# Kernel optimization log

Hardware: AMD Instinct MI355X
Metric: run time of the kernel (lower is better)

The kernel has to match this reference:

```python
import jax, jax.numpy as jnp
import numpy as np

N, E = 50000, 800000
IN_DIM, HEADS, OUT_DIM = 256, 8, 32
NEG_SLOPE = 0.2  # PyG GATConv default leaky_relu slope
LN_EPS = 1e-5


def setup_inputs() -> dict:
    key = jax.random.key(0)
    ks = jax.random.split(key, 8)
    HC = HEADS * OUT_DIM
    x = jax.random.normal(ks[0], (N, IN_DIM), dtype=jnp.float32)
    edge_index = jax.random.randint(ks[1], (2, E), 0, N, dtype=jnp.int32)
    # GATConv params: lin (no bias), att_src/att_dst [H,C], output bias [H*C]
    W = jax.random.normal(ks[2], (IN_DIM, HC), dtype=jnp.float32) / np.sqrt(IN_DIM)
    att_src = jax.random.normal(ks[3], (HEADS, OUT_DIM), dtype=jnp.float32) / np.sqrt(OUT_DIM)
    att_dst = jax.random.normal(ks[4], (HEADS, OUT_DIM), dtype=jnp.float32) / np.sqrt(OUT_DIM)
    bias = jnp.zeros((HC,), dtype=jnp.float32)
    ln_gamma = jnp.ones((HC,), dtype=jnp.float32)
    ln_beta = jnp.zeros((HC,), dtype=jnp.float32)
    return {"x": x, "edge_index": edge_index, "W": W, "att_src": att_src,
            "att_dst": att_dst, "bias": bias, "ln_gamma": ln_gamma, "ln_beta": ln_beta}


def reference(x, edge_index, W, att_src, att_dst, bias, ln_gamma, ln_beta):
    n = x.shape[0]
    # GATConv adds self-loops by default
    loop = jnp.arange(n, dtype=edge_index.dtype)
    src = jnp.concatenate([edge_index[0], loop])  # [E+N]
    dst = jnp.concatenate([edge_index[1], loop])
    h = (x @ W).reshape(n, HEADS, OUT_DIM)              # [N,H,C]
    a_src = jnp.einsum('nhc,hc->nh', h, att_src)        # [N,H]
    a_dst = jnp.einsum('nhc,hc->nh', h, att_dst)
    e = jax.nn.leaky_relu(a_src[src] + a_dst[dst], NEG_SLOPE)  # [E+N,H]
    # segment-softmax over incoming edges of each destination node
    m = jax.ops.segment_max(e, dst, num_segments=n)
    e = jnp.exp(e - m[dst])
    denom = jax.ops.segment_sum(e, dst, num_segments=n)
    alpha = e / (denom[dst] + 1e-16)                    # [E+N,H]
    out = jax.ops.segment_sum(h[src] * alpha[:, :, None], dst, num_segments=n)
    out = out.reshape(n, HEADS * OUT_DIM) + bias        # concat heads + bias
    # LayerNorm(out_dim*heads); dropout is identity in eval
    mu = jnp.mean(out, axis=-1, keepdims=True)
    var = jnp.mean(jnp.square(out - mu), axis=-1, keepdims=True)
    return ln_gamma * (out - mu) * jax.lax.rsqrt(var + LN_EPS) + ln_beta
```

## Files before the change

### kernel.cpp

```cpp
#include <hip/hip_runtime.h>

#define HEADS 8
#define OUT_DIM 32
#define HC 256
#define IN_DIM 256
#define NEG_SLOPE 0.2f
#define LN_EPS 1e-5f
#define CAP 64

typedef __attribute__((ext_vector_type(8))) short bf16x8;
typedef __attribute__((ext_vector_type(4))) float f32x4;
typedef __attribute__((ext_vector_type(2))) float f32x2;

__device__ __forceinline__ unsigned short f2bf(float f) {
    unsigned int u = __float_as_uint(f);
    unsigned int r = u + 0x7FFFu + ((u >> 16) & 1u);
    return (unsigned short)(r >> 16);
}
__device__ __forceinline__ float bf2f(unsigned short u) {
    return __uint_as_float((unsigned int)u << 16);
}

__global__ __launch_bounds__(256) void cast_wT(const float* __restrict__ W,
                                               unsigned short* __restrict__ Wt) {
    __shared__ float tile[64][65];
    const int n0 = (blockIdx.x & 3) * 64;
    const int k0 = (blockIdx.x >> 2) * 64;
    const int t = threadIdx.x;
    const int r = t >> 4;
    const int c = (t & 15) * 4;
#pragma unroll
    for (int j = 0; j < 4; j++) {
        const int kl = r + j * 16;
        const float4 v = *(const float4*)(W + (size_t)(k0 + kl) * HC + n0 + c);
        tile[kl][c + 0] = v.x; tile[kl][c + 1] = v.y;
        tile[kl][c + 2] = v.z; tile[kl][c + 3] = v.w;
    }
    __syncthreads();
#pragma unroll
    for (int j = 0; j < 4; j++) {
        const int nr = r + j * 16;
        ushort4 o;
        o.x = f2bf(tile[c + 0][nr]);
        o.y = f2bf(tile[c + 1][nr]);
        o.z = f2bf(tile[c + 2][nr]);
        o.w = f2bf(tile[c + 3][nr]);
        *(ushort4*)(Wt + (size_t)(n0 + nr) * IN_DIM + k0 + c) = o;
    }
}

__global__ __launch_bounds__(256) void gemm_bf16(const float* __restrict__ X,
                                                 const unsigned short* __restrict__ Wt,
                                                 unsigned short* __restrict__ Hb,
                                                 const float* __restrict__ att_s,
                                                 const float* __restrict__ att_d,
                                                 float* __restrict__ a_s,
                                                 float* __restrict__ a_d, int M) {
    __shared__ unsigned short smem[128 * 40 + 256 * 40];
    unsigned short* As = smem;
    unsigned short* Bs = smem + 128 * 40;
    const int t = threadIdx.x;
    const int m0 = blockIdx.x * 128;
    const int w = t >> 6, lane = t & 63;
    const int wr = w >> 1, wn = w & 1;
    const int l16 = lane & 15, quad = lane >> 4;

    f32x4 acc[4][8] = {};

    for (int k0 = 0; k0 < IN_DIM; k0 += 32) {
#pragma unroll
        for (int j = 0; j < 4; j++) {
            const int idx = t + j * 256;
            const int row = idx >> 3;
            const int part = idx & 7;
            float4 v = make_float4(0.f, 0.f, 0.f, 0.f);
            const int gm = m0 + row;
            if (gm < M) v = *(const float4*)(X + (size_t)gm * IN_DIM + k0 + part * 4);
            ushort4 b;
            b.x = f2bf(v.x); b.y = f2bf(v.y); b.z = f2bf(v.z); b.w = f2bf(v.w);
            *(ushort4*)&As[row * 40 + part * 4] = b;
        }
#pragma unroll
        for (int j = 0; j < 4; j++) {
            const int idx = t + j * 256;
            const int n = idx >> 2;
            const int part = idx & 3;
            *(uint4*)&Bs[n * 40 + part * 8] =
                *(const uint4*)(Wt + (size_t)n * IN_DIM + k0 + part * 8);
        }
        __syncthreads();

        bf16x8 af[4];
#pragma unroll
        for (int mi = 0; mi < 4; mi++) {
            const int row = wr * 64 + mi * 16 + l16;
            af[mi] = *(const bf16x8*)&As[row * 40 + quad * 8];
        }
#pragma unroll
        for (int ni = 0; ni < 8; ni++) {
            const int col = wn * 128 + ni * 16 + l16;
            const bf16x8 bfr = *(const bf16x8*)&Bs[col * 40 + quad * 8];
#pragma unroll
            for (int mi = 0; mi < 4; mi++)
                acc[mi][ni] = __builtin_amdgcn_mfma_f32_16x16x32_bf16(af[mi], bfr, acc[mi][ni], 0, 0, 0);
        }
        __syncthreads();
    }

    {
        float as_v[8], ad_v[8];
#pragma unroll
        for (int ni = 0; ni < 8; ni++) {
            as_v[ni] = att_s[wn * 128 + ni * 16 + l16];
            ad_v[ni] = att_d[wn * 128 + ni * 16 + l16];
        }
#pragma unroll
        for (int mi = 0; mi < 4; mi++) {
#pragma unroll
            for (int reg = 0; reg < 4; reg++) {
                float ps0 = acc[mi][0][reg] * as_v[0] + acc[mi][1][reg] * as_v[1];
                float ps1 = acc[mi][2][reg] * as_v[2] + acc[mi][3][reg] * as_v[3];
                float ps2 = acc[mi][4][reg] * as_v[4] + acc[mi][5][reg] * as_v[5];
                float ps3 = acc[mi][6][reg] * as_v[6] + acc[mi][7][reg] * as_v[7];
                float pd0 = acc[mi][0][reg] * ad_v[0] + acc[mi][1][reg] * ad_v[1];
                float pd1 = acc[mi][2][reg] * ad_v[2] + acc[mi][3][reg] * ad_v[3];
                float pd2 = acc[mi][4][reg] * ad_v[4] + acc[mi][5][reg] * ad_v[5];
                float pd3 = acc[mi][6][reg] * ad_v[6] + acc[mi][7][reg] * ad_v[7];
#pragma unroll
                for (int m = 1; m <= 2; m <<= 1) {
                    ps0 += __shfl_xor(ps0, m); ps1 += __shfl_xor(ps1, m);
                    ps2 += __shfl_xor(ps2, m); ps3 += __shfl_xor(ps3, m);
                    pd0 += __shfl_xor(pd0, m); pd1 += __shfl_xor(pd1, m);
                    pd2 += __shfl_xor(pd2, m); pd3 += __shfl_xor(pd3, m);
                }
                const int s2 = l16 & 3;
                float vs = s2 == 0 ? ps0 : (s2 == 1 ? ps1 : (s2 == 2 ? ps2 : ps3));
                float vd = s2 == 0 ? pd0 : (s2 == 1 ? pd1 : (s2 == 2 ? pd2 : pd3));
                vs += __shfl_xor(vs, 4); vs += __shfl_xor(vs, 8);
                vd += __shfl_xor(vd, 4); vd += __shfl_xor(vd, 8);
                const int gm = m0 + wr * 64 + mi * 16 + quad * 4 + reg;
                if (l16 < 4 && gm < M) {
                    a_s[(size_t)gm * HEADS + wn * 4 + l16] = vs;
                    a_d[(size_t)gm * HEADS + wn * 4 + l16] = vd;
                }
            }
        }
    }

    unsigned short* cbuf = smem + w * 2048;
#pragma unroll
    for (int mi = 0; mi < 4; mi++) {
#pragma unroll
        for (int ni = 0; ni < 8; ni++) {
#pragma unroll
            for (int reg = 0; reg < 4; reg++) {
                cbuf[(quad * 4 + reg) * 128 + ni * 16 + l16] = f2bf(acc[mi][ni][reg]);
            }
        }
#pragma unroll
        for (int j = 0; j < 4; j++) {
            const int q = lane + 64 * j;
            const int r = q >> 4;
            const int cc = q & 15;
            const uint4 v = *(const uint4*)&cbuf[r * 128 + cc * 8];
            const int gm = m0 + wr * 64 + mi * 16 + r;
            if (gm < M)
                *(uint4*)(Hb + (size_t)gm * HC + wn * 128 + cc * 8) = v;
        }
    }
}

__global__ __launch_bounds__(256) void bucket_scatter(const int* __restrict__ ei,
                                                      int* __restrict__ cnt,
                                                      int* __restrict__ bucket,
                                                      int E, int N) {
    const int e = blockIdx.x * 256 + threadIdx.x;
    if (e >= E + N) return;
    int s, d;
    if (e < E) { s = ei[e]; d = ei[E + e]; }
    else       { s = d = e - E; }
    int slot = atomicAdd(&cnt[d], 1);
    if (slot < CAP) bucket[(size_t)d * CAP + slot] = s;
}

__global__ __launch_bounds__(256) void csr_agg(const int* __restrict__ cntArr,
                                               const int* __restrict__ bucket,
                                               const unsigned short* __restrict__ Hb,
                                               const float* __restrict__ a_s,
                                               const float* __restrict__ a_d,
                                               const float* __restrict__ bias,
                                               const float* __restrict__ gamma,
                                               const float* __restrict__ beta,
                                               float* __restrict__ out, int N) {
    const int lane = threadIdx.x & 63;
    const int node = blockIdx.x * 4 + (threadIdx.x >> 6);
    if (node >= N) return;
    const int half = lane >> 5;
    const int sl   = lane & 31;
    const int c0   = sl * 8;
    const int hh   = sl >> 2;
    const int base = node * CAP;
    const int cnt  = min(cntArr[node], CAP);
    const float adv = a_d[(size_t)node * HEADS + hh];
    const int breg = bucket[base + lane];

    f32x2 acc2[4] = {};
    float wsum = 0.f;

    const int nIter = (cnt + 7) >> 3;

    int   sv[4];  float tl[4];  float msk[4];  uint4 hv[4];
#pragma unroll
    for (int j = 0; j < 4; j++) {
        const int idx = 2 * j + half;
        const int s = __shfl(breg, idx);
        const bool ok = idx < cnt;
        sv[j]  = ok ? s : 0;
        msk[j] = ok ? 1.f : 0.f;
    }
#pragma unroll
    for (int j = 0; j < 4; j++) tl[j] = a_s[(size_t)sv[j] * HEADS + hh];
#pragma unroll
    for (int j = 0; j < 4; j++) hv[j] = *(const uint4*)(Hb + (size_t)sv[j] * HC + c0);

    for (int it = 0; it < nIter; ++it) {
        int   sv2[4]; float tl2[4]; float msk2[4]; uint4 hv2[4];
        const int i2 = (it + 1) * 8;
#pragma unroll
        for (int j = 0; j < 4; j++) {
            const int idx = i2 + 2 * j + half;
            const int s = __shfl(breg, idx & 63);
            const bool ok = idx < cnt;
            sv2[j]  = ok ? s : 0;
            msk2[j] = ok ? 1.f : 0.f;
        }
#pragma unroll
        for (int j = 0; j < 4; j++) tl2[j] = a_s[(size_t)sv2[j] * HEADS + hh];
#pragma unroll
        for (int j = 0; j < 4; j++) hv2[j] = *(const uint4*)(Hb + (size_t)sv2[j] * HC + c0);

#pragma unroll
        for (int j = 0; j < 4; j++) {
            const float t = tl[j] + adv;
            const float l = fmaxf(t, NEG_SLOPE * t);
            const float w = msk[j] * __expf(l);
            wsum += w;
            f32x2 wv; wv.x = w; wv.y = w;
            f32x2 p0, p1, p2, p3;
            p0.x = __uint_as_float(hv[j].x << 16); p0.y = __uint_as_float(hv[j].x & 0xffff0000u);
            p1.x = __uint_as_float(hv[j].y << 16); p1.y = __uint_as_float(hv[j].y & 0xffff0000u);
            p2.x = __uint_as_float(hv[j].z << 16); p2.y = __uint_as_float(hv[j].z & 0xffff0000u);
            p3.x = __uint_as_float(hv[j].w << 16); p3.y = __uint_as_float(hv[j].w & 0xffff0000u);
            acc2[0] += wv * p0;
            acc2[1] += wv * p1;
            acc2[2] += wv * p2;
            acc2[3] += wv * p3;
        }
#pragma unroll
        for (int j = 0; j < 4; j++) { tl[j] = tl2[j]; msk[j] = msk2[j]; hv[j] = hv2[j]; }
    }

    float acc[8];
    acc[0] = acc2[0].x; acc[1] = acc2[0].y; acc[2] = acc2[1].x; acc[3] = acc2[1].y;
    acc[4] = acc2[2].x; acc[5] = acc2[2].y; acc[6] = acc2[3].x; acc[7] = acc2[3].y;

#pragma unroll
    for (int k = 0; k < 8; k++) acc[k] += __shfl_xor(acc[k], 32);
    wsum += __shfl_xor(wsum, 32);

    const float inv = 1.f / (wsum + 1e-16f);
    const float4 b0 = *(const float4*)(bias + c0);
    const float4 b1 = *(const float4*)(bias + c0 + 4);
    float v[8];
    v[0] = acc[0] * inv + b0.x; v[1] = acc[1] * inv + b0.y;
    v[2] = acc[2] * inv + b0.z; v[3] = acc[3] * inv + b0.w;
    v[4] = acc[4] * inv + b1.x; v[5] = acc[5] * inv + b1.y;
    v[6] = acc[6] * inv + b1.z; v[7] = acc[7] * inv + b1.w;

    float s1 = v[0] + v[1] + v[2] + v[3] + v[4] + v[5] + v[6] + v[7];
#pragma unroll
    for (int m = 1; m < 64; m <<= 1) s1 += __shfl_xor(s1, m);
    const float mu = s1 * (1.f / 512.f);
    float d[8];
    float sq = 0.f;
#pragma unroll
    for (int k = 0; k < 8; k++) { d[k] = v[k] - mu; sq += d[k] * d[k]; }
#pragma unroll
    for (int m = 1; m < 64; m <<= 1) sq += __shfl_xor(sq, m);
    const float rs = rsqrtf(sq * (1.f / 512.f) + LN_EPS);

    const float e0 = half ? d[4] : d[0];
    const float e1 = half ? d[5] : d[1];
    const float e2 = half ? d[6] : d[2];
    const float e3 = half ? d[7] : d[3];
    const int co = c0 + half * 4;
    const float4 g  = *(const float4*)(gamma + co);
    const float4 be = *(const float4*)(beta + co);
    float4 o;
    o.x = g.x * e0 * rs + be.x;
    o.y = g.y * e1 * rs + be.y;
    o.z = g.z * e2 * rs + be.z;
    o.w = g.w * e3 * rs + be.w;
    *(float4*)(out + (size_t)node * HC + co) = o;
}

extern "C" void kernel_launch(void* const* d_in, const int* in_sizes, int n_in,
                              void* d_out, int out_size, void* d_ws, size_t ws_size,
                              hipStream_t stream) {
    const float* x     = (const float*)d_in[0];
    const int*   ei    = (const int*)d_in[1];
    const float* W     = (const float*)d_in[2];
    const float* att_s = (const float*)d_in[3];
    const float* att_d = (const float*)d_in[4];
    const float* bias  = (const float*)d_in[5];
    const float* gamma = (const float*)d_in[6];
    const float* beta  = (const float*)d_in[7];
    float* out = (float*)d_out;

    const int N = in_sizes[0] / IN_DIM;
    const int E = in_sizes[1] / 2;
    const int tot = E + N;

    unsigned short* Hb = (unsigned short*)d_ws;
    unsigned short* Wt = Hb + (size_t)N * HC;
    float* a_s  = (float*)(Wt + (size_t)IN_DIM * HC);
    float* a_d  = a_s + (size_t)N * HEADS;
    int* cnt    = (int*)(a_d + (size_t)N * HEADS);
    int* bucket = cnt + N;

    hipMemsetAsync(cnt, 0, (size_t)N * sizeof(int), stream);

    bucket_scatter<<<(tot + 255) / 256, 256, 0, stream>>>(ei, cnt, bucket, E, N);
    cast_wT<<<16, 256, 0, stream>>>(W, Wt);
    gemm_bf16<<<(N + 127) / 128, 256, 0, stream>>>(x, Wt, Hb, att_s, att_d, a_s, a_d, N);

    csr_agg<<<(N + 3) / 4, 256, 0, stream>>>(cnt, bucket, Hb, a_s, a_d,
                                             bias, gamma, beta, out, N);
}
```

Before: 287.1 us.

## Drop LDS staging in GEMM and compute attention logits in separate kernel

The GEMM now loads X and W fragments straight from global memory into MFMA registers with no shared memory or barriers, uses 64-row tiles with 4 waves each covering 64 columns, and writes bf16 H directly. The attention dot products a_s and a_d move out of the GEMM epilogue into a new node_att kernel that rereads the bf16 H. This aims to cut barrier and LDS overhead and register pressure to raise occupancy. The cost is redundant global loads of X across waves, uncoalesced scalar stores of H, an extra launch, and logits computed from bf16-rounded H rather than fp32 accumulators.

```diff
diff --git a/kernel.cpp b/kernel.cpp
--- a/kernel.cpp
+++ b/kernel.cpp
@@ -1,4 +1,5 @@
 #include <hip/hip_runtime.h>
+#include <hip/hip_bf16.h>
 
 #define HEADS 8
 #define OUT_DIM 32
@@ -19,6 +20,20 @@
 }
 __device__ __forceinline__ float bf2f(unsigned short u) {
     return __uint_as_float((unsigned int)u << 16);
+}
+
+__device__ __forceinline__ unsigned short f2bf_hw(float f) {
+    union { __hip_bfloat16 h; unsigned short u; } c;
+    c.h = __float2bfloat16(f);
+    return c.u;
+}
+__device__ __forceinline__ bf16x8 pack8(const float4 a, const float4 b) {
+    bf16x8 r;
+    r[0] = (short)f2bf_hw(a.x); r[1] = (short)f2bf_hw(a.y);
+    r[2] = (short)f2bf_hw(a.z); r[3] = (short)f2bf_hw(a.w);
+    r[4] = (short)f2bf_hw(b.x); r[5] = (short)f2bf_hw(b.y);
+    r[6] = (short)f2bf_hw(b.z); r[7] = (short)f2bf_hw(b.w);
+    return r;
 }
 
 __global__ __launch_bounds__(256) void cast_wT(const float* __restrict__ W,
@@ -49,124 +64,94 @@
     }
 }
 
-__global__ __launch_bounds__(256) void gemm_bf16(const float* __restrict__ X,
-                                                 const unsigned short* __restrict__ Wt,
-                                                 unsigned short* __restrict__ Hb,
-                                                 const float* __restrict__ att_s,
-                                                 const float* __restrict__ att_d,
-                                                 float* __restrict__ a_s,
-                                                 float* __restrict__ a_d, int M) {
-    __shared__ unsigned short smem[128 * 40 + 256 * 40];
-    unsigned short* As = smem;
-    unsigned short* Bs = smem + 128 * 40;
+__global__ __launch_bounds__(256, 3) void gemm_bf16(const float* __restrict__ X,
+                                                    const unsigned short* __restrict__ Wt,
+                                                    unsigned short* __restrict__ Hb, int M) {
     const int t = threadIdx.x;
-    const int m0 = blockIdx.x * 128;
     const int w = t >> 6, lane = t & 63;
-    const int wr = w >> 1, wn = w & 1;
     const int l16 = lane & 15, quad = lane >> 4;
-
-    f32x4 acc[4][8] = {};
-
+    const int m0 = blockIdx.x * 64;
+    const int n0 = w * 64;
+
+    const float* xp[4];
+#pragma unroll
+    for (int mi = 0; mi < 4; mi++) {
+        const int gm = m0 + mi * 16 + l16;
+        xp[mi] = X + (size_t)(gm < M ? gm : 0) * IN_DIM + quad * 8;
+    }
+    const unsigned short* bp[4];
+#pragma unroll
+    for (int ni = 0; ni < 4; ni++)
+        bp[ni] = Wt + (size_t)(n0 + ni * 16 + l16) * IN_DIM + quad * 8;
+
+    f32x4 acc[4][4] = {};
+
+#pragma unroll
     for (int k0 = 0; k0 < IN_DIM; k0 += 32) {
-#pragma unroll
-        for (int j = 0; j < 4; j++) {
-            const int idx = t + j * 256;
-            const int row = idx >> 3;
-            const int part = idx & 7;
-            float4 v = make_float4(0.f, 0.f, 0.f, 0.f);
-            const int gm = m0 + row;
-            if (gm < M) v = *(const float4*)(X + (size_t)gm * IN_DIM + k0 + part * 4);
-            ushort4 b;
-            b.x = f2bf(v.x); b.y = f2bf(v.y); b.z = f2bf(v.z); b.w = f2bf(v.w);
-            *(ushort4*)&As[row * 40 + part * 4] = b;
+        bf16x8 bfr[4];
+#pragma unroll
+        for (int ni = 0; ni < 4; ni++)
+            bfr[ni] = *(const bf16x8*)(bp[ni] + k0);
+        bf16x8 af[4];
+#pragma unroll
+        for (int mi = 0; mi < 4; mi++) {
+            const float4 a0 = *(const float4*)(xp[mi] + k0);
+            const float4 a1 = *(const float4*)(xp[mi] + k0 + 4);
+            af[mi] = pack8(a0, a1);
         }
 #pragma unroll
-        for (int j = 0; j < 4; j++) {
-            const int idx = t + j * 256;
-            const int n = idx >> 2;
-            const int part = idx & 3;
-            *(uint4*)&Bs[n * 40 + part * 8] =
-                *(const uint4*)(Wt + (size_t)n * IN_DIM + k0 + part * 8);
-        }
-        __syncthreads();
-
-        bf16x8 af[4];
-#pragma unroll
-        for (int mi = 0; mi < 4; mi++) {
-            const int row = wr * 64 + mi * 16 + l16;
-            af[mi] = *(const bf16x8*)&As[row * 40 + quad * 8];
-        }
-#pragma unroll
-        for (int ni = 0; ni < 8; ni++) {
-            const int col = wn * 128 + ni * 16 + l16;
-            const bf16x8 bfr = *(const bf16x8*)&Bs[col * 40 + quad * 8];
+        for (int ni = 0; ni < 4; ni++)
 #pragma unroll
             for (int mi = 0; mi < 4; mi++)
-                acc[mi][ni] = __builtin_amdgcn_mfma_f32_16x16x32_bf16(af[mi], bfr, acc[mi][ni], 0, 0, 0);
-        }
-        __syncthreads();
-    }
-
-    {
-        float as_v[8], ad_v[8];
-#pragma unroll
-        for (int ni = 0; ni < 8; ni++) {
-            as_v[ni] = att_s[wn * 128 + ni * 16 + l16];
-            ad_v[ni] = att_d[wn * 128 + ni * 16 + l16];
-        }
-#pragma unroll
-        for (int mi = 0; mi < 4; mi++) {
-#pragma unroll
-            for (int reg = 0; reg < 4; reg++) {
-                float ps0 = acc[mi][0][reg] * as_v[0] + acc[mi][1][reg] * as_v[1];
-                float ps1 = acc[mi][2][reg] * as_v[2] + acc[mi][3][reg] * as_v[3];
-                float ps2 = acc[mi][4][reg] * as_v[4] + acc[mi][5][reg] * as_v[5];
-                float ps3 = acc[mi][6][reg] * as_v[6] + acc[mi][7][reg] * as_v[7];
-                float pd0 = acc[mi][0][reg] * ad_v[0] + acc[mi][1][reg] * ad_v[1];
-                float pd1 = acc[mi][2][reg] * ad_v[2] + acc[mi][3][reg] * ad_v[3];
-                float pd2 = acc[mi][4][reg] * ad_v[4] + acc[mi][5][reg] * ad_v[5];
-                float pd3 = acc[mi][6][reg] * ad_v[6] + acc[mi][7][reg] * ad_v[7];
-#pragma unroll
-                for (int m = 1; m <= 2; m <<= 1) {
-                    ps0 += __shfl_xor(ps0, m); ps1 += __shfl_xor(ps1, m);
-                    ps2 += __shfl_xor(ps2, m); ps3 += __shfl_xor(ps3, m);
-                    pd0 += __shfl_xor(pd0, m); pd1 += __shfl_xor(pd1, m);
-                    pd2 += __shfl_xor(pd2, m); pd3 += __shfl_xor(pd3, m);
-                }
-                const int s2 = l16 & 3;
-                float vs = s2 == 0 ? ps0 : (s2 == 1 ? ps1 : (s2 == 2 ? ps2 : ps3));
-                float vd = s2 == 0 ? pd0 : (s2 == 1 ? pd1 : (s2 == 2 ? pd2 : pd3));
-                vs += __shfl_xor(vs, 4); vs += __shfl_xor(vs, 8);
-                vd += __shfl_xor(vd, 4); vd += __shfl_xor(vd, 8);
-                const int gm = m0 + wr * 64 + mi * 16 + quad * 4 + reg;
-                if (l16 < 4 && gm < M) {
-                    a_s[(size_t)gm * HEADS + wn * 4 + l16] = vs;
-                    a_d[(size_t)gm * HEADS + wn * 4 + l16] = vd;
-                }
+                acc[mi][ni] = __builtin_amdgcn_mfma_f32_16x16x32_bf16(af[mi], bfr[ni], acc[mi][ni], 0, 0, 0);
+    }
+
+#pragma unroll
+    for (int mi = 0; mi < 4; mi++) {
+#pragma unroll
+        for (int reg = 0; reg < 4; reg++) {
+            const int gm = m0 + mi * 16 + quad * 4 + reg;
+            if (gm < M) {
+#pragma unroll
+                for (int ni = 0; ni < 4; ni++)
+                    Hb[(size_t)gm * HC + n0 + ni * 16 + l16] = f2bf(acc[mi][ni][reg]);
             }
         }
     }
-
-    unsigned short* cbuf = smem + w * 2048;
-#pragma unroll
-    for (int mi = 0; mi < 4; mi++) {
-#pragma unroll
-        for (int ni = 0; ni < 8; ni++) {
-#pragma unroll
-            for (int reg = 0; reg < 4; reg++) {
-                cbuf[(quad * 4 + reg) * 128 + ni * 16 + l16] = f2bf(acc[mi][ni][reg]);
-            }
-        }
-#pragma unroll
-        for (int j = 0; j < 4; j++) {
-            const int q = lane + 64 * j;
-            const int r = q >> 4;
-            const int cc = q & 15;
-            const uint4 v = *(const uint4*)&cbuf[r * 128 + cc * 8];
-            const int gm = m0 + wr * 64 + mi * 16 + r;
-            if (gm < M)
-                *(uint4*)(Hb + (size_t)gm * HC + wn * 128 + cc * 8) = v;
-        }
+}
+
+__global__ __launch_bounds__(256) void node_att(const unsigned short* __restrict__ Hb,
+                                                const float* __restrict__ att_s,
+                                                const float* __restrict__ att_d,
+                                                float* __restrict__ a_s,
+                                                float* __restrict__ a_d, int N) {
+    const int lane = threadIdx.x & 63;
+    const int wv   = threadIdx.x >> 6;
+    const int half = lane >> 5;
+    const int sl   = lane & 31;
+    const int node = blockIdx.x * 8 + wv * 2 + half;
+    if (node >= N) return;
+    const int c0 = sl * 8;
+    const int hh = sl >> 2;
+    const uint4 hv = *(const uint4*)(Hb + (size_t)node * HC + c0);
+    float h[8];
+    h[0] = __uint_as_float(hv.x << 16); h[1] = __uint_as_float(hv.x & 0xffff0000u);
+    h[2] = __uint_as_float(hv.y << 16); h[3] = __uint_as_float(hv.y & 0xffff0000u);
+    h[4] = __uint_as_float(hv.z << 16); h[5] = __uint_as_float(hv.z & 0xffff0000u);
+    h[6] = __uint_as_float(hv.w << 16); h[7] = __uint_as_float(hv.w & 0xffff0000u);
+    const float4 s0 = *(const float4*)(att_s + c0);
+    const float4 s1 = *(const float4*)(att_s + c0 + 4);
+    const float4 d0 = *(const float4*)(att_d + c0);
+    const float4 d1 = *(const float4*)(att_d + c0 + 4);
+    float ps = h[0]*s0.x + h[1]*s0.y + h[2]*s0.z + h[3]*s0.w
+             + h[4]*s1.x + h[5]*s1.y + h[6]*s1.z + h[7]*s1.w;
+    float pd = h[0]*d0.x + h[1]*d0.y + h[2]*d0.z + h[3]*d0.w
+             + h[4]*d1.x + h[5]*d1.y + h[6]*d1.z + h[7]*d1.w;
+    ps += __shfl_xor(ps, 1); ps += __shfl_xor(ps, 2);
+    pd += __shfl_xor(pd, 1); pd += __shfl_xor(pd, 2);
+    if ((sl & 3) == 0) {
+        a_s[node * HEADS + hh] = ps;
+        a_d[node * HEADS + hh] = pd;
     }
 }
 
@@ -332,7 +317,8 @@
 
     bucket_scatter<<<(tot + 255) / 256, 256, 0, stream>>>(ei, cnt, bucket, E, N);
     cast_wT<<<16, 256, 0, stream>>>(W, Wt);
-    gemm_bf16<<<(N + 127) / 128, 256, 0, stream>>>(x, Wt, Hb, att_s, att_d, a_s, a_d, N);
+    gemm_bf16<<<(N + 63) / 64, 256, 0, stream>>>(x, Wt, Hb, N);
+    node_att<<<(N + 7) / 8, 256, 0, stream>>>(Hb, att_s, att_d, a_s, a_d, N);
 
     csr_agg<<<(N + 3) / 4, 256, 0, stream>>>(cnt, bucket, Hb, a_s, a_d,
                                              bias, gamma, beta, out, N);
```

Measured after the change: 282.7 us. About the same (-1.5%).
